# Optimization experiments

Hardware: AMD Instinct MI355X
Metric: run time of the kernel (lower is better)

## Reference

```python
import jax, jax.numpy as jnp
import numpy as np

B, D, H, O, E, R, K, NH = 2048, 512, 2048, 512, 8, 4, 2, 8
DH = O // NH
EPS = 1e-5

def _ln(x, g, b):
    m = x.mean(-1, keepdims=True)
    v = ((x - m) ** 2).mean(-1, keepdims=True)
    return (x - m) / jnp.sqrt(v + EPS) * g + b

def setup_inputs():
    key = jax.random.key(0)
    ks = jax.random.split(key, 16)
    n = lambda k, shape, fan: jax.random.normal(k, shape, jnp.float32) * (fan ** -0.5)
    x = jax.random.normal(ks[0], (B, D), jnp.float32)
    regime = jax.random.randint(ks[1], (B,), 0, R)
    regime_features = jax.nn.one_hot(regime, R, dtype=jnp.float32)
    return dict(
        x=x, regime=regime, regime_features=regime_features,
        ew1=n(ks[2], (R, E, D, H), D), eb1=jnp.zeros((R, E, H)),
        lng=jnp.ones((R, E, H)), lnb=jnp.zeros((R, E, H)),
        ew2=n(ks[3], (R, E, H, O), H), eb2=jnp.zeros((R, E, O)),
        rw1=n(ks[4], (R, D + R, H), D + R), rb1=jnp.zeros((R, H)),
        rw2=n(ks[5], (R, H, E), H), rb2=jnp.zeros((R, E)),
        ipw=n(ks[6], (3 * O, O), O), ipb=jnp.zeros((3 * O,)),
        opw=n(ks[7], (O, O), O), opb=jnp.zeros((O,)),
        ang=jnp.ones((O,)), anb=jnp.zeros((O,)),
    )

def _forward(x, regime, regime_features, ew1, eb1, lng, lnb, ew2, eb2, rw1, rb1, rw2, rb2, ipw, ipb, opw, opb, ang, anb):
    B_ = x.shape[0]
    bi = jnp.arange(B_)
    # regime-conditioned routing: compute logits for all regimes densely, select per sample
    ri = jnp.concatenate([x, regime_features], axis=-1)                  # [B, D+R]
    rh = jax.nn.relu(jnp.einsum('bf,rfh->rbh', ri, rw1) + rb1[:, None])
    logits = (jnp.einsum('rbh,rhe->rbe', rh, rw2) + rb2[:, None])[regime, bi]  # [B, E]
    w = jax.nn.softmax(logits, axis=-1)
    tkw, tki = jax.lax.top_k(w, K)
    tkw = tkw / tkw.sum(-1, keepdims=True)
    # experts: all regimes x all experts, then select the per-sample regime block
    h = jnp.einsum('bd,redh->rebh', x, ew1) + eb1[:, :, None]            # [R, E, B, H]
    h = jax.nn.relu(_ln(h, lng[:, :, None], lnb[:, :, None]))
    eo = jnp.einsum('rebh,reho->rebo', h, ew2) + eb2[:, :, None] + x[None, None]  # identity residual (D == O)
    eo = eo.transpose(0, 2, 1, 3)[regime, bi]                            # [B, E, O]
    # group attention over expert axis (torch MultiheadAttention, eval mode)
    qkv = eo @ ipw.T + ipb
    q, k, v = jnp.split(qkv, 3, axis=-1)
    sh = lambda t: t.reshape(B_, E, NH, DH).transpose(0, 2, 1, 3)
    q, k, v = sh(q), sh(k), sh(v)
    attn = jax.nn.softmax(jnp.einsum('bhqd,bhkd->bhqk', q, k) / np.sqrt(DH).astype(np.float32), axis=-1)
    av = jnp.einsum('bhqk,bhkd->bhqd', attn, v).transpose(0, 2, 1, 3).reshape(B_, E, O)
    eo = _ln(eo + av @ opw.T + opb, ang, anb)
    # top-k combine
    gathered = jnp.take_along_axis(eo, tki[:, :, None], axis=1)          # [B, K, O]
    return jnp.sum(tkw[:, :, None] * gathered, axis=1)

def reference(x, regime, regime_features, ew1, eb1, lng, lnb, ew2, eb2, rw1, rb1, rw2, rb2, ipw, ipb, opw, opb, ang, anb):
    return _forward(x, regime, regime_features, ew1, eb1, lng, lnb, ew2, eb2, rw1, rb1, rw2, rb2, ipw, ipb, opw, opb, ang, anb)
```

## Files before the change

kernel.cpp:

```cpp
#include <hip/hip_runtime.h>
#include <hip/hip_bf16.h>
#include <cstddef>

typedef __attribute__((ext_vector_type(8))) short short8;
typedef __attribute__((ext_vector_type(4))) float f32x4;

constexpr int CB = 2048;
constexpr int CD = 512;
constexpr int CH = 2048;
constexpr int CO = 512;
constexpr int CE = 8;
constexpr int CR = 4;

__device__ __forceinline__ float bs2f(short s){
  union { float f; unsigned u; } u; u.u = ((unsigned)(unsigned short)s) << 16; return u.f;
}
__device__ __forceinline__ short f2bs(float x){
  union { __hip_bfloat16 h; short s; } u; u.h = __float2bfloat16(x); return u.s;
}

#define GLL(g, l) __builtin_amdgcn_global_load_lds((const __attribute__((address_space(1))) void*)(g), (__attribute__((address_space(3))) void*)(l), 16, 0, 0)

__device__ __forceinline__ void block_reduce2(float& a, float& b){
#pragma unroll
  for (int off = 32; off; off >>= 1){ a += __shfl_xor(a, off, 64); b += __shfl_xor(b, off, 64); }
  __shared__ float sa[4], sb[4];
  const int wid = threadIdx.x >> 6, lane = threadIdx.x & 63;
  __syncthreads();
  if (lane == 0){ sa[wid] = a; sb[wid] = b; }
  __syncthreads();
  a = sa[0] + sa[1] + sa[2] + sa[3];
  b = sb[0] + sb[1] + sb[2] + sb[3];
}

__global__ void k_count(const int* __restrict__ regime, int* __restrict__ meta){
  int b = blockIdx.x * 256 + threadIdx.x;
  if (b < CB) atomicAdd(&meta[8 + regime[b]], 1);
}
__global__ void k_scan(int* meta){
  if (threadIdx.x == 0){
    int c0 = meta[8], c1 = meta[9], c2 = meta[10], c3 = meta[11];
    meta[0] = 0; meta[1] = c0; meta[2] = c0 + c1; meta[3] = c0 + c1 + c2; meta[4] = c0 + c1 + c2 + c3;
  }
}
__global__ void k_scatter(const int* __restrict__ regime, int* __restrict__ meta, int* __restrict__ perm){
  int b = blockIdx.x * 256 + threadIdx.x;
  if (b < CB){
    int r = regime[b];
    int pos = atomicAdd(&meta[12 + r], 1);
    perm[meta[r] + pos] = b;
  }
}

__global__ __launch_bounds__(256) void k_xsplit(const float* __restrict__ x, const int* __restrict__ perm,
                                                short* __restrict__ xp, short* __restrict__ xd){
  const int i = blockIdx.x;
  const int b = perm[i];
  const int c = threadIdx.x * 2;
  float2 v = *(const float2*)(x + (size_t)b * CD + c);
  short2 hi; hi.x = f2bs(v.x); hi.y = f2bs(v.y);
  short2 lo; lo.x = f2bs(v.x - bs2f(hi.x)); lo.y = f2bs(v.y - bs2f(hi.y));
  *(short2*)(xp + (size_t)i * CD + c) = hi;
  short* row = xd + (size_t)i * 2048;
  *(short2*)(row + c) = hi;
  *(short2*)(row + 512 + c) = hi;
  *(short2*)(row + 1024 + c) = lo;
  *(short2*)(row + 1536 + c) = lo;
}

__global__ __launch_bounds__(256) void k_cvt(const float* __restrict__ in, short* __restrict__ outp, int n){
  int i = (blockIdx.x * 256 + threadIdx.x) * 8;
  if (i >= n) return;
  float4 a = *(const float4*)(in + i);
  float4 b = *(const float4*)(in + i + 4);
  short8 o;
  o[0]=f2bs(a.x); o[1]=f2bs(a.y); o[2]=f2bs(a.z); o[3]=f2bs(a.w);
  o[4]=f2bs(b.x); o[5]=f2bs(b.y); o[6]=f2bs(b.z); o[7]=f2bs(b.w);
  *(short8*)(outp + i) = o;
}

__global__ __launch_bounds__(256) void k_cvt_t(const float* __restrict__ in, short* __restrict__ outp, int K, int N){
  __shared__ float tile[64][65];
  const int z = blockIdx.z;
  const int k0 = blockIdx.y * 64, n0 = blockIdx.x * 64;
  const float* src = in + (size_t)z * K * N;
  short* dst = outp + (size_t)z * K * N;
  const int t = threadIdx.x;
  const int kk = t >> 4, nq = (t & 15) * 4;
#pragma unroll
  for (int j = 0; j < 4; j++){
    float4 v = *(const float4*)(src + (size_t)(k0 + kk + j * 16) * N + n0 + nq);
    tile[kk + j * 16][nq] = v.x; tile[kk + j * 16][nq + 1] = v.y;
    tile[kk + j * 16][nq + 2] = v.z; tile[kk + j * 16][nq + 3] = v.w;
  }
  __syncthreads();
  const int n = t >> 2, kq = (t & 3) * 16;
  short8 o0, o1;
#pragma unroll
  for (int j = 0; j < 8; j++) o0[j] = f2bs(tile[kq + j][n]);
#pragma unroll
  for (int j = 0; j < 8; j++) o1[j] = f2bs(tile[kq + 8 + j][n]);
  short* drow = dst + (size_t)(n0 + n) * K + k0 + kq;
  *(short8*)(drow) = o0;
  *(short8*)(drow + 8) = o1;
}

__global__ __launch_bounds__(256) void k_rwt(const float* __restrict__ rw1, short* __restrict__ Bp){
  __shared__ float tile[64][65];
  const int r = blockIdx.z;
  const int k0 = blockIdx.y * 64, n0 = blockIdx.x * 64;
  const float* src = rw1 + (size_t)r * (CD + CR) * CH;
  short* dst = Bp + (size_t)r * CH * 2048;
  const int t = threadIdx.x;
  const int kk = t >> 4, nq = (t & 15) * 4;
#pragma unroll
  for (int j = 0; j < 4; j++){
    float4 v = *(const float4*)(src + (size_t)(k0 + kk + j * 16) * CH + n0 + nq);
    tile[kk + j * 16][nq] = v.x; tile[kk + j * 16][nq + 1] = v.y;
    tile[kk + j * 16][nq + 2] = v.z; tile[kk + j * 16][nq + 3] = v.w;
  }
  __syncthreads();
  const int n = t >> 2, kq = (t & 3) * 16;
  short8 h0, h1, l0, l1;
#pragma unroll
  for (int j = 0; j < 8; j++){
    float f = tile[kq + j][n];
    short h = f2bs(f); h0[j] = h; l0[j] = f2bs(f - bs2f(h));
  }
#pragma unroll
  for (int j = 0; j < 8; j++){
    float f = tile[kq + 8 + j][n];
    short h = f2bs(f); h1[j] = h; l1[j] = f2bs(f - bs2f(h));
  }
  short* drow = dst + (size_t)(n0 + n) * 2048;
  *(short8*)(drow + k0 + kq) = h0;        *(short8*)(drow + k0 + kq + 8) = h1;
  *(short8*)(drow + 512 + k0 + kq) = l0;  *(short8*)(drow + 512 + k0 + kq + 8) = l1;
  *(short8*)(drow + 1024 + k0 + kq) = h0; *(short8*)(drow + 1024 + k0 + kq + 8) = h1;
  *(short8*)(drow + 1536 + k0 + kq) = l0; *(short8*)(drow + 1536 + k0 + kq + 8) = l1;
}

__global__ void k_rbias(const float* __restrict__ rw1, const float* __restrict__ rb1, float* __restrict__ rbias){
  const int r = blockIdx.y, n = blockIdx.x * 256 + threadIdx.x;
  rbias[r * CH + n] = rb1[(size_t)r * CH + n] + rw1[((size_t)r * (CD + CR) + CD + r) * CH + n];
}

__global__ __launch_bounds__(256) void k_logits2(
    const float* __restrict__ part, const float* __restrict__ rb2,
    const int* __restrict__ meta, const int* __restrict__ perm,
    int* __restrict__ tki, float* __restrict__ tkw){
  const int wid = threadIdx.x >> 6, lane = threadIdx.x & 63;
  const int i = blockIdx.x * 4 + wid;
  const int r = (i >= meta[1]) + (i >= meta[2]) + (i >= meta[3]);
  const int p0 = lane >> 3, e = lane & 7;
  float v = 0.f;
#pragma unroll
  for (int j = 0; j < 4; j++)
    v += part[((size_t)(p0 + 8 * j) * CB + i) * 8 + e];
  v += __shfl_xor(v, 8, 64);
  v += __shfl_xor(v, 16, 64);
  v += __shfl_xor(v, 32, 64);
  v += rb2[r * CE + e];
  float l8[8];
#pragma unroll
  for (int e2 = 0; e2 < 8; e2++) l8[e2] = __shfl(v, e2, 64);
  if (lane == 0){
    int i1 = 0; float m1 = l8[0];
#pragma unroll
    for (int e2 = 1; e2 < 8; e2++) if (l8[e2] > m1){ m1 = l8[e2]; i1 = e2; }
    int i2 = -1; float m2 = -1e30f;
#pragma unroll
    for (int e2 = 0; e2 < 8; e2++) if (e2 != i1 && l8[e2] > m2){ m2 = l8[e2]; i2 = e2; }
    const float e2w = __expf(m2 - m1);
    const float w1 = 1.f / (1.f + e2w);
    const int b = perm[i];
    tki[b * 2] = i1; tki[b * 2 + 1] = i2;
    tkw[b * 2] = w1; tkw[b * 2 + 1] = e2w * w1;
  }
}
__global__ void k_qrows(const int* __restrict__ tki, int* __restrict__ qrows){
  int i = blockIdx.x * 256 + threadIdx.x;
  if (i < CB * 2) qrows[i] = (i >> 1) * CE + tki[i];
}

template<int EPI, bool SWZ>
__global__ __launch_bounds__(256) void gemm_bf16(
    const short* __restrict__ A, long lda,
    const short* __restrict__ Wt, long ldw,
    const int* __restrict__ goff, int fixedM, int Ksub, int ksplit, int N,
    const float* __restrict__ bias, long bstride,
    short* __restrict__ outb, short* __restrict__ outb2, float* __restrict__ outf,
    const int* __restrict__ operm, const float* __restrict__ xtra, int mbs, int nbs){
  constexpr int BK = 32;
  __shared__ __align__(16) short lds[2][8192];

  int bx, by, bz;
  if constexpr (SWZ){
    const int s = blockIdx.x;
    const int chunk = gridDim.x >> 3;
    const int l = (s & 7) * chunk + (s >> 3);
    bx = l % nbs; const int t2 = l / nbs; by = t2 % mbs; bz = t2 / mbs;
  } else { bx = blockIdx.x; by = blockIdx.y; bz = blockIdx.z; }

  const int ks = bz % ksplit;
  const int z = bz / ksplit;
  int g0 = 0, Mg = fixedM;
  if (goff){ const int r = (EPI == 6) ? z : (z >> 3); g0 = goff[r]; Mg = goff[r + 1] - g0; }
  const int m0 = by * 128;
  if (m0 >= Mg) return;
  const int n0 = bx * 128;
  const int e = z & 7;
  const long kbase = (long)ks * Ksub;

  const short* Ab;
  if constexpr (EPI == 2) Ab = A + ((size_t)e * CB + g0) * (size_t)lda;
  else if constexpr (EPI == 1 || EPI == 6) Ab = A + (size_t)g0 * (size_t)lda;
  else Ab = A;
  const short* Wb = Wt + (size_t)z * (size_t)N * (size_t)ldw;

  const int tid = threadIdx.x;
  const int lane = tid & 63, wid = tid >> 6;
  const int srow = lane >> 2;
  const int sc = (((lane & 3) ^ ((srow >> 1) & 3)) << 3);

  int ar0 = m0 + wid * 32 + srow;
  int ar1 = ar0 + 16;
  if (ar0 > Mg - 1) ar0 = Mg - 1;
  if (ar1 > Mg - 1) ar1 = Mg - 1;
  if constexpr (EPI == 3){
    if (operm){ ar0 = operm[ar0]; ar1 = operm[ar1]; }
  }
  const short* ga0 = Ab + (size_t)ar0 * lda + kbase + sc;
  const short* ga1 = Ab + (size_t)ar1 * lda + kbase + sc;
  const int brow = n0 + wid * 32 + srow;
  const short* gb0 = Wb + (size_t)brow * ldw + kbase + sc;
  const short* gb1 = gb0 + (size_t)16 * ldw;

  const int wm = (wid >> 1) * 64, wn = (wid & 1) * 64;
  const int r16 = lane & 15, kb = lane >> 4;
  const int rsw = (r16 >> 1) & 3;

  f32x4 acc[4][4];
#pragma unroll
  for (int a = 0; a < 4; a++)
#pragma unroll
    for (int b = 0; b < 4; b++) acc[a][b] = (f32x4){0.f, 0.f, 0.f, 0.f};

  const int NT = Ksub / BK;
  int buf = 0;

  {
    short* dA = &lds[0][0] + wid * 1024;
    short* dB = &lds[0][4096] + wid * 1024;
    GLL(ga0, dA); GLL(ga1, dA + 512);
    GLL(gb0, dB); GLL(gb1, dB + 512);
  }
  __syncthreads();

  for (int t = 0; t < NT; ++t){
    if (t + 1 < NT){
      const int kof = (t + 1) * BK;
      short* dA = &lds[buf ^ 1][0] + wid * 1024;
      short* dB = &lds[buf ^ 1][4096] + wid * 1024;
      GLL(ga0 + kof, dA); GLL(ga1 + kof, dA + 512);
      GLL(gb0 + kof, dB); GLL(gb1 + kof, dB + 512);
    }
    const short* sA = &lds[buf][0];
    const short* sB = &lds[buf][4096];
    short8 af[4], bfv[4];
#pragma unroll
    for (int mi = 0; mi < 4; mi++)
      af[mi] = *(const short8*)(sA + (wm + mi * 16 + r16) * 32 + ((kb ^ rsw) << 3));
#pragma unroll
    for (int ni = 0; ni < 4; ni++)
      bfv[ni] = *(const short8*)(sB + (wn + ni * 16 + r16) * 32 + ((kb ^ rsw) << 3));
#pragma unroll
    for (int mi = 0; mi < 4; mi++)
#pragma unroll
      for (int ni = 0; ni < 4; ni++)
        acc[mi][ni] = __builtin_amdgcn_mfma_f32_16x16x32_bf16(af[mi], bfv[ni], acc[mi][ni], 0, 0, 0);
    __syncthreads();
    buf ^= 1;
  }

  if constexpr (EPI == 6){
    const int hbase = n0 + wn;
    float wv[4][8]; float rbv[4];
#pragma unroll
    for (int ni = 0; ni < 4; ni++){
      const int h = hbase + ni * 16 + r16;
      rbv[ni] = bias[(size_t)z * CH + h];
      const float* wp = xtra + ((size_t)z * CH + h) * 8;
#pragma unroll
      for (int e2 = 0; e2 < 8; e2++) wv[ni][e2] = wp[e2];
    }
    const int slot = bx * 2 + (wid & 1);
#pragma unroll
    for (int mi = 0; mi < 4; mi++){
#pragma unroll
      for (int q = 0; q < 4; q++){
        float tmp[8];
#pragma unroll
        for (int e2 = 0; e2 < 8; e2++) tmp[e2] = 0.f;
#pragma unroll
        for (int ni = 0; ni < 4; ni++){
          const float v = fmaxf(acc[mi][ni][q] + rbv[ni], 0.f);
#pragma unroll
          for (int e2 = 0; e2 < 8; e2++) tmp[e2] += v * wv[ni][e2];
        }
#pragma unroll
        for (int e2 = 0; e2 < 8; e2++){
          tmp[e2] += __shfl_xor(tmp[e2], 1, 64);
          tmp[e2] += __shfl_xor(tmp[e2], 2, 64);
          tmp[e2] += __shfl_xor(tmp[e2], 4, 64);
          tmp[e2] += __shfl_xor(tmp[e2], 8, 64);
        }
        const int row = wm + mi * 16 + kb * 4 + q;
        if (r16 == 0 && m0 + row < Mg){
          float* dp = outf + ((size_t)slot * CB + (g0 + m0 + row)) * 8;
#pragma unroll
          for (int e2 = 0; e2 < 8; e2++) dp[e2] = tmp[e2];
        }
      }
    }
    return;
  }

#pragma unroll
  for (int mi = 0; mi < 4; mi++){
#pragma unroll
    for (int q = 0; q < 4; q++){
      const int i = m0 + wm + mi * 16 + kb * 4 + q;
      if (i >= Mg) continue;
#pragma unroll
      for (int ni = 0; ni < 4; ni++){
        const int n = n0 + wn + ni * 16 + r16;
        float v = acc[mi][ni][q];
        if constexpr (EPI == 1){
          v += bias[(size_t)z * bstride + n];
          outb[((size_t)e * CB + (g0 + i)) * (size_t)N + n] = f2bs(v);
        } else if constexpr (EPI == 2){
          const int borig = operm[g0 + i];
          short* tgt = ks ? outb2 : outb;
          tgt[((size_t)borig * CE + e) * (size_t)CO + n] = f2bs(v);
        } else if constexpr (EPI == 3){
          v += bias[n];
          outb[(size_t)i * (size_t)N + n] = f2bs(v);
        } else {
          v += bias[n];
          outf[(size_t)i * (size_t)N + n] = v;
        }
      }
    }
  }
}

__global__ __launch_bounds__(256) void k_eo(const short* __restrict__ p1,
    const float* __restrict__ eb2, const float* __restrict__ x, const int* __restrict__ regime,
    short* __restrict__ eo){
  const int b = blockIdx.x, e = blockIdx.y;
  const int r = regime[b];
  const int c = threadIdx.x * 2;
  const size_t idx = (((size_t)b * CE + e) << 9) + c;
  short2 a = *(const short2*)(eo + idx);
  short2 bb = *(const short2*)(p1 + idx);
  float2 xr = *(const float2*)(x + (size_t)b * CD + c);
  float2 eb = *(const float2*)(eb2 + (((size_t)r * CE + e) << 9) + c);
  short2 o;
  o.x = f2bs(bs2f(a.x) + bs2f(bb.x) + xr.x + eb.x);
  o.y = f2bs(bs2f(a.y) + bs2f(bb.y) + xr.y + eb.y);
  *(short2*)(eo + idx) = o;
}

__global__ __launch_bounds__(256) void k_ln(short* __restrict__ hact,
    const float* __restrict__ lng, const float* __restrict__ lnb, const int* __restrict__ meta){
  const int rowid = blockIdx.x;
  const int e = rowid >> 11, i = rowid & (CB - 1);
  const int r = (i >= meta[1]) + (i >= meta[2]) + (i >= meta[3]);
  short* p = hact + (size_t)rowid * CH;
  short8 raw = *(short8*)(p + threadIdx.x * 8);
  float v[8]; float s = 0.f, sq = 0.f;
#pragma unroll
  for (int j = 0; j < 8; j++){ v[j] = bs2f(raw[j]); s += v[j]; sq += v[j] * v[j]; }
  block_reduce2(s, sq);
  const float mean = s * (1.f / CH);
  const float var = sq * (1.f / CH) - mean * mean;
  const float rstd = rsqrtf(fmaxf(var, 0.f) + 1e-5f);
  const float* g = lng + ((size_t)r * CE + e) * CH;
  const float* bb = lnb + ((size_t)r * CE + e) * CH;
  short8 outv;
#pragma unroll
  for (int j = 0; j < 8; j++){
    const int h = threadIdx.x * 8 + j;
    const float val = (v[j] - mean) * rstd * g[h] + bb[h];
    outv[j] = f2bs(fmaxf(val, 0.f));
  }
  *(short8*)(p + threadIdx.x * 8) = outv;
}

__global__ __launch_bounds__(128) void k_attn(const short* __restrict__ qb, const short* __restrict__ kv,
    const int* __restrict__ tki, short* __restrict__ av){
  const int b = blockIdx.x;
  const int j = threadIdx.x >> 6, d = threadIdx.x & 63;
  const short* q = qb + (size_t)(b * 2 + j) * CO;
  const short* base = kv + (size_t)b * CE * 1024;
#pragma unroll
  for (int h = 0; h < 8; h++){
    const float qv = bs2f(q[h * 64 + d]);
    float sc[8];
#pragma unroll
    for (int e = 0; e < 8; e++){
      float pp = qv * bs2f(base[(size_t)e * 1024 + h * 64 + d]);
#pragma unroll
      for (int off = 32; off; off >>= 1) pp += __shfl_xor(pp, off, 64);
      sc[e] = pp * 0.125f;
    }
    float m = sc[0];
#pragma unroll
    for (int e = 1; e < 8; e++) m = fmaxf(m, sc[e]);
    float den = 0.f, avd = 0.f;
#pragma unroll
    for (int e = 0; e < 8; e++){
      const float pe = __expf(sc[e] - m);
      den += pe;
      avd += pe * bs2f(base[(size_t)e * 1024 + 512 + h * 64 + d]);
    }
    av[((size_t)b * 2 + j) * CO + h * 64 + d] = f2bs(avd / den);
  }
}

__global__ __launch_bounds__(256) void k_final(const short* __restrict__ eo,
    const float* __restrict__ proj, const int* __restrict__ tki, const float* __restrict__ tkw,
    const float* __restrict__ ang, const float* __restrict__ anb, float* __restrict__ out){
  const int b = blockIdx.x, t = threadIdx.x;
  float o0 = 0.f, o1 = 0.f;
#pragma unroll
  for (int j = 0; j < 2; j++){
    const int s = tki[b * 2 + j];
    const float w = tkw[b * 2 + j];
    const short* ep = eo + ((size_t)b * CE + s) * CO;
    const float* pp = proj + ((size_t)b * 2 + j) * CO;
    const float v0 = bs2f(ep[t]) + pp[t];
    const float v1 = bs2f(ep[t + 256]) + pp[t + 256];
    float sm = v0 + v1, sq = v0 * v0 + v1 * v1;
    block_reduce2(sm, sq);
    const float mean = sm * (1.f / CO);
    const float rstd = rsqrtf(fmaxf(sq * (1.f / CO) - mean * mean, 0.f) + 1e-5f);
    o0 += w * ((v0 - mean) * rstd * ang[t] + anb[t]);
    o1 += w * ((v1 - mean) * rstd * ang[t + 256] + anb[t + 256]);
  }
  out[(size_t)b * CO + t] = o0;
  out[(size_t)b * CO + t + 256] = o1;
}

extern "C" void kernel_launch(void* const* d_in, const int* in_sizes, int n_in,
                              void* d_out, int out_size, void* d_ws, size_t ws_size,
                              hipStream_t stream){
  const float* x    = (const float*)d_in[0];
  const int*   regime = (const int*)d_in[1];
  const float* ew1  = (const float*)d_in[3];
  const float* eb1  = (const float*)d_in[4];
  const float* lng  = (const float*)d_in[5];
  const float* lnb  = (const float*)d_in[6];
  const float* ew2  = (const float*)d_in[7];
  const float* eb2  = (const float*)d_in[8];
  const float* rw1  = (const float*)d_in[9];
  const float* rb1  = (const float*)d_in[10];
  const float* rw2  = (const float*)d_in[11];
  const float* rb2  = (const float*)d_in[12];
  const float* ipw  = (const float*)d_in[13];
  const float* ipb  = (const float*)d_in[14];
  const float* opw  = (const float*)d_in[15];
  const float* opb  = (const float*)d_in[16];
  const float* ang  = (const float*)d_in[17];
  const float* anb  = (const float*)d_in[18];
  float* out = (float*)d_out;

  char* ws = (char*)d_ws;
  int*   meta  = (int*)(ws);
  int*   perm  = (int*)(ws + (16u << 10));
  int*   tki   = (int*)(ws + (32u << 10));
  float* tkw   = (float*)(ws + (48u << 10));
  int*   qrows = (int*)(ws + (64u << 10));
  float* rbias = (float*)(ws + (80u << 10));
  short* ipwb  = (short*)(ws + (256u << 10));
  short* opwb  = (short*)(ws + (1792u << 10));
  short* xp    = (short*)(ws + (2304u << 10));
  short* eo    = (short*)(ws + (4352u << 10));
  short* hact  = (short*)(ws + (22ull << 20));
  short* qkv   = (short*)(ws + (22ull << 20));
  short* qb    = (short*)(ws + (54ull << 20));
  short* av    = (short*)(ws + (58ull << 20));
  float* proj  = (float*)(ws + (62ull << 20));
  float* part  = (float*)(ws + (70ull << 20));
  short* wt    = (short*)(ws + (86ull << 20));
  short* xd    = (short*)(ws + (150ull << 20));
  short* p1    = (short*)(ws + (150ull << 20));

  hipMemsetAsync(meta, 0, 1024, stream);
  k_count  <<<8, 256, 0, stream>>>(regime, meta);
  k_scan   <<<1, 64, 0, stream>>>(meta);
  k_scatter<<<8, 256, 0, stream>>>(regime, meta, perm);
  k_xsplit <<<CB, 256, 0, stream>>>(x, perm, xp, xd);
  k_cvt    <<<384, 256, 0, stream>>>(ipw, ipwb, 1536 * 512);
  k_cvt    <<<128, 256, 0, stream>>>(opw, opwb, 512 * 512);

  k_rwt  <<<dim3(32, 8, CR), 256, 0, stream>>>(rw1, wt);
  k_rbias<<<dim3(8, CR), 256, 0, stream>>>(rw1, rb1, rbias);
  gemm_bf16<6, false><<<dim3(16, 16, CR), 256, 0, stream>>>(
      xd, 2048, wt, 2048, meta, 0, 2048, 1, CH, rbias, 0,
      nullptr, nullptr, part, nullptr, rw2, 0, 0);
  k_logits2<<<CB / 4, 256, 0, stream>>>(part, rb2, meta, perm, tki, tkw);
  k_qrows<<<16, 256, 0, stream>>>(tki, qrows);

  k_cvt_t<<<dim3(32, 8, 32), 256, 0, stream>>>(ew1, wt, CD, CH);
  gemm_bf16<1, true><<<8192, 256, 0, stream>>>(
      xp, CD, wt, CD, meta, 0, CD, 1, CH, eb1, CH, hact, nullptr, nullptr, nullptr, nullptr, 16, 16);
  k_ln<<<CE * CB, 256, 0, stream>>>(hact, lng, lnb, meta);

  k_cvt_t<<<dim3(8, 32, 32), 256, 0, stream>>>(ew2, wt, CH, CO);
  gemm_bf16<2, true><<<4096, 256, 0, stream>>>(
      hact, CH, wt, CH, meta, 0, 1024, 2, CO, nullptr, 0, eo, p1, nullptr, perm, nullptr, 16, 4);
  k_eo<<<dim3(CB, CE), 256, 0, stream>>>(p1, eb2, x, regime, eo);

  gemm_bf16<3, true><<<1024, 256, 0, stream>>>(
      eo, CO, ipwb + (size_t)512 * 512, CO, nullptr, CB * CE, CO, 1, 1024, ipb + 512, 0,
      qkv, nullptr, nullptr, nullptr, nullptr, 128, 8);
  gemm_bf16<3, false><<<dim3(4, 32, 1), 256, 0, stream>>>(
      eo, CO, ipwb, CO, nullptr, CB * 2, CO, 1, CO, ipb, 0,
      qb, nullptr, nullptr, qrows, nullptr, 0, 0);

  k_attn<<<CB, 128, 0, stream>>>(qb, qkv, tki, av);

  gemm_bf16<4, false><<<dim3(4, 32, 1), 256, 0, stream>>>(
      av, CO, opwb, CO, nullptr, CB * 2, CO, 1, CO, opb, 0,
      nullptr, nullptr, proj, nullptr, nullptr, 0, 0);

  k_final<<<CB, 256, 0, stream>>>(eo, proj, tki, tkw, ang, anb, out);
  (void)in_sizes; (void)n_in; (void)out_size; (void)ws_size;
}
```

Before: 441.2 us.

## Drop lo*lo split term in router GEMM, split-K 4 for expert GEMM2, fuse small kernels

The router GEMM's split-bf16 emulation shrinks from four terms to three by dropping the lo*lo product, so K goes from 2048 to 1536. The second expert GEMM now uses split-K of 4 instead of 2, and all partials go to separate buffers that k_eo sums. Several small launches are merged: the two weight casts become one kernel, the bias computation moves into k_rwt, and qrows is written in k_logits2. This saves GEMM work and launches but writes and reads more partial-sum traffic, and slightly lowers router precision.

```diff
diff --git a/kernel.cpp b/kernel.cpp
--- a/kernel.cpp
+++ b/kernel.cpp
@@ -61,22 +61,24 @@
   short2 hi; hi.x = f2bs(v.x); hi.y = f2bs(v.y);
   short2 lo; lo.x = f2bs(v.x - bs2f(hi.x)); lo.y = f2bs(v.y - bs2f(hi.y));
   *(short2*)(xp + (size_t)i * CD + c) = hi;
-  short* row = xd + (size_t)i * 2048;
+  short* row = xd + (size_t)i * 1536;
   *(short2*)(row + c) = hi;
   *(short2*)(row + 512 + c) = hi;
   *(short2*)(row + 1024 + c) = lo;
-  *(short2*)(row + 1536 + c) = lo;
-}
-
-__global__ __launch_bounds__(256) void k_cvt(const float* __restrict__ in, short* __restrict__ outp, int n){
+}
+
+__global__ __launch_bounds__(256) void k_cvt2(const float* __restrict__ a, short* __restrict__ ao, int na,
+                                              const float* __restrict__ b, short* __restrict__ bo, int nb){
   int i = (blockIdx.x * 256 + threadIdx.x) * 8;
-  if (i >= n) return;
-  float4 a = *(const float4*)(in + i);
-  float4 b = *(const float4*)(in + i + 4);
+  const float* src; short* dst;
+  if (i < na){ src = a + i; dst = ao + i; }
+  else { int j = i - na; if (j >= nb) return; src = b + j; dst = bo + j; }
+  float4 u = *(const float4*)(src);
+  float4 v = *(const float4*)(src + 4);
   short8 o;
-  o[0]=f2bs(a.x); o[1]=f2bs(a.y); o[2]=f2bs(a.z); o[3]=f2bs(a.w);
-  o[4]=f2bs(b.x); o[5]=f2bs(b.y); o[6]=f2bs(b.z); o[7]=f2bs(b.w);
-  *(short8*)(outp + i) = o;
+  o[0]=f2bs(u.x); o[1]=f2bs(u.y); o[2]=f2bs(u.z); o[3]=f2bs(u.w);
+  o[4]=f2bs(v.x); o[5]=f2bs(v.y); o[6]=f2bs(v.z); o[7]=f2bs(v.w);
+  *(short8*)(dst) = o;
 }
 
 __global__ __launch_bounds__(256) void k_cvt_t(const float* __restrict__ in, short* __restrict__ outp, int K, int N){
@@ -105,13 +107,18 @@
   *(short8*)(drow + 8) = o1;
 }
 
-__global__ __launch_bounds__(256) void k_rwt(const float* __restrict__ rw1, short* __restrict__ Bp){
+__global__ __launch_bounds__(256) void k_rwt(const float* __restrict__ rw1, const float* __restrict__ rb1,
+                                             short* __restrict__ Bp, float* __restrict__ rbias){
   __shared__ float tile[64][65];
   const int r = blockIdx.z;
   const int k0 = blockIdx.y * 64, n0 = blockIdx.x * 64;
   const float* src = rw1 + (size_t)r * (CD + CR) * CH;
-  short* dst = Bp + (size_t)r * CH * 2048;
+  short* dst = Bp + (size_t)r * CH * 1536;
   const int t = threadIdx.x;
+  if (blockIdx.y == 0 && t < 64){
+    const int n = n0 + t;
+    rbias[r * CH + n] = rb1[(size_t)r * CH + n] + src[((size_t)(CD + r)) * CH + n];
+  }
   const int kk = t >> 4, nq = (t & 15) * 4;
 #pragma unroll
   for (int j = 0; j < 4; j++){
@@ -132,22 +139,16 @@
     float f = tile[kq + 8 + j][n];
     short h = f2bs(f); h1[j] = h; l1[j] = f2bs(f - bs2f(h));
   }
-  short* drow = dst + (size_t)(n0 + n) * 2048;
+  short* drow = dst + (size_t)(n0 + n) * 1536;
   *(short8*)(drow + k0 + kq) = h0;        *(short8*)(drow + k0 + kq + 8) = h1;
   *(short8*)(drow + 512 + k0 + kq) = l0;  *(short8*)(drow + 512 + k0 + kq + 8) = l1;
   *(short8*)(drow + 1024 + k0 + kq) = h0; *(short8*)(drow + 1024 + k0 + kq + 8) = h1;
-  *(short8*)(drow + 1536 + k0 + kq) = l0; *(short8*)(drow + 1536 + k0 + kq + 8) = l1;
-}
-
-__global__ void k_rbias(const float* __restrict__ rw1, const float* __restrict__ rb1, float* __restrict__ rbias){
-  const int r = blockIdx.y, n = blockIdx.x * 256 + threadIdx.x;
-  rbias[r * CH + n] = rb1[(size_t)r * CH + n] + rw1[((size_t)r * (CD + CR) + CD + r) * CH + n];
 }
 
 __global__ __launch_bounds__(256) void k_logits2(
     const float* __restrict__ part, const float* __restrict__ rb2,
     const int* __restrict__ meta, const int* __restrict__ perm,
-    int* __restrict__ tki, float* __restrict__ tkw){
+    int* __restrict__ tki, float* __restrict__ tkw, int* __restrict__ qrows){
   const int wid = threadIdx.x >> 6, lane = threadIdx.x & 63;
   const int i = blockIdx.x * 4 + wid;
   const int r = (i >= meta[1]) + (i >= meta[2]) + (i >= meta[3]);
@@ -175,11 +176,8 @@
     const int b = perm[i];
     tki[b * 2] = i1; tki[b * 2 + 1] = i2;
     tkw[b * 2] = w1; tkw[b * 2 + 1] = e2w * w1;
-  }
-}
-__global__ void k_qrows(const int* __restrict__ tki, int* __restrict__ qrows){
-  int i = blockIdx.x * 256 + threadIdx.x;
-  if (i < CB * 2) qrows[i] = (i >> 1) * CE + tki[i];
+    qrows[b * 2] = b * CE + i1; qrows[b * 2 + 1] = b * CE + i2;
+  }
 }
 
 template<int EPI, bool SWZ>
@@ -188,7 +186,7 @@
     const short* __restrict__ Wt, long ldw,
     const int* __restrict__ goff, int fixedM, int Ksub, int ksplit, int N,
     const float* __restrict__ bias, long bstride,
-    short* __restrict__ outb, short* __restrict__ outb2, float* __restrict__ outf,
+    short* __restrict__ outb, float* __restrict__ outf,
     const int* __restrict__ operm, const float* __restrict__ xtra, int mbs, int nbs){
   constexpr int BK = 32;
   __shared__ __align__(16) short lds[2][8192];
@@ -340,8 +338,7 @@
           outb[((size_t)e * CB + (g0 + i)) * (size_t)N + n] = f2bs(v);
         } else if constexpr (EPI == 2){
           const int borig = operm[g0 + i];
-          short* tgt = ks ? outb2 : outb;
-          tgt[((size_t)borig * CE + e) * (size_t)CO + n] = f2bs(v);
+          outb[(size_t)ks * bstride + ((size_t)borig * CE + e) * (size_t)CO + n] = f2bs(v);
         } else if constexpr (EPI == 3){
           v += bias[n];
           outb[(size_t)i * (size_t)N + n] = f2bs(v);
@@ -354,20 +351,22 @@
   }
 }
 
-__global__ __launch_bounds__(256) void k_eo(const short* __restrict__ p1,
+__global__ __launch_bounds__(256) void k_eo(const short* __restrict__ P, long pstr,
     const float* __restrict__ eb2, const float* __restrict__ x, const int* __restrict__ regime,
     short* __restrict__ eo){
   const int b = blockIdx.x, e = blockIdx.y;
   const int r = regime[b];
   const int c = threadIdx.x * 2;
   const size_t idx = (((size_t)b * CE + e) << 9) + c;
-  short2 a = *(const short2*)(eo + idx);
-  short2 bb = *(const short2*)(p1 + idx);
+  short2 a0 = *(const short2*)(P + idx);
+  short2 a1 = *(const short2*)(P + pstr + idx);
+  short2 a2 = *(const short2*)(P + 2 * pstr + idx);
+  short2 a3 = *(const short2*)(P + 3 * pstr + idx);
   float2 xr = *(const float2*)(x + (size_t)b * CD + c);
   float2 eb = *(const float2*)(eb2 + (((size_t)r * CE + e) << 9) + c);
   short2 o;
-  o.x = f2bs(bs2f(a.x) + bs2f(bb.x) + xr.x + eb.x);
-  o.y = f2bs(bs2f(a.y) + bs2f(bb.y) + xr.y + eb.y);
+  o.x = f2bs(bs2f(a0.x) + bs2f(a1.x) + bs2f(a2.x) + bs2f(a3.x) + xr.x + eb.x);
+  o.y = f2bs(bs2f(a0.y) + bs2f(a1.y) + bs2f(a2.y) + bs2f(a3.y) + xr.y + eb.y);
   *(short2*)(eo + idx) = o;
 }
 
@@ -493,47 +492,45 @@
   float* proj  = (float*)(ws + (62ull << 20));
   float* part  = (float*)(ws + (70ull << 20));
   short* wt    = (short*)(ws + (86ull << 20));
-  short* xd    = (short*)(ws + (150ull << 20));
-  short* p1    = (short*)(ws + (150ull << 20));
+  short* P     = (short*)(ws + (150ull << 20));
+  short* xd    = (short*)(ws + (216ull << 20));
+  const long PSTR = (long)CB * CE * CO;
 
   hipMemsetAsync(meta, 0, 1024, stream);
   k_count  <<<8, 256, 0, stream>>>(regime, meta);
   k_scan   <<<1, 64, 0, stream>>>(meta);
   k_scatter<<<8, 256, 0, stream>>>(regime, meta, perm);
   k_xsplit <<<CB, 256, 0, stream>>>(x, perm, xp, xd);
-  k_cvt    <<<384, 256, 0, stream>>>(ipw, ipwb, 1536 * 512);
-  k_cvt    <<<128, 256, 0, stream>>>(opw, opwb, 512 * 512);
-
-  k_rwt  <<<dim3(32, 8, CR), 256, 0, stream>>>(rw1, wt);
-  k_rbias<<<dim3(8, CR), 256, 0, stream>>>(rw1, rb1, rbias);
+  k_cvt2   <<<512, 256, 0, stream>>>(ipw, ipwb, 1536 * 512, opw, opwb, 512 * 512);
+
+  k_rwt<<<dim3(32, 8, CR), 256, 0, stream>>>(rw1, rb1, wt, rbias);
   gemm_bf16<6, false><<<dim3(16, 16, CR), 256, 0, stream>>>(
-      xd, 2048, wt, 2048, meta, 0, 2048, 1, CH, rbias, 0,
-      nullptr, nullptr, part, nullptr, rw2, 0, 0);
-  k_logits2<<<CB / 4, 256, 0, stream>>>(part, rb2, meta, perm, tki, tkw);
-  k_qrows<<<16, 256, 0, stream>>>(tki, qrows);
+      xd, 1536, wt, 1536, meta, 0, 1536, 1, CH, rbias, 0,
+      nullptr, part, nullptr, rw2, 0, 0);
+  k_logits2<<<CB / 4, 256, 0, stream>>>(part, rb2, meta, perm, tki, tkw, qrows);
 
   k_cvt_t<<<dim3(32, 8, 32), 256, 0, stream>>>(ew1, wt, CD, CH);
   gemm_bf16<1, true><<<8192, 256, 0, stream>>>(
-      xp, CD, wt, CD, meta, 0, CD, 1, CH, eb1, CH, hact, nullptr, nullptr, nullptr, nullptr, 16, 16);
+      xp, CD, wt, CD, meta, 0, CD, 1, CH, eb1, CH, hact, nullptr, nullptr, nullptr, 16, 16);
   k_ln<<<CE * CB, 256, 0, stream>>>(hact, lng, lnb, meta);
 
   k_cvt_t<<<dim3(8, 32, 32), 256, 0, stream>>>(ew2, wt, CH, CO);
-  gemm_bf16<2, true><<<4096, 256, 0, stream>>>(
-      hact, CH, wt, CH, meta, 0, 1024, 2, CO, nullptr, 0, eo, p1, nullptr, perm, nullptr, 16, 4);
-  k_eo<<<dim3(CB, CE), 256, 0, stream>>>(p1, eb2, x, regime, eo);
+  gemm_bf16<2, true><<<8192, 256, 0, stream>>>(
+      hact, CH, wt, CH, meta, 0, 512, 4, CO, nullptr, PSTR, P, nullptr, perm, nullptr, 16, 4);
+  k_eo<<<dim3(CB, CE), 256, 0, stream>>>(P, PSTR, eb2, x, regime, eo);
 
   gemm_bf16<3, true><<<1024, 256, 0, stream>>>(
       eo, CO, ipwb + (size_t)512 * 512, CO, nullptr, CB * CE, CO, 1, 1024, ipb + 512, 0,
-      qkv, nullptr, nullptr, nullptr, nullptr, 128, 8);
+      qkv, nullptr, nullptr, nullptr, 128, 8);
   gemm_bf16<3, false><<<dim3(4, 32, 1), 256, 0, stream>>>(
       eo, CO, ipwb, CO, nullptr, CB * 2, CO, 1, CO, ipb, 0,
-      qb, nullptr, nullptr, qrows, nullptr, 0, 0);
+      qb, nullptr, qrows, nullptr, 0, 0);
 
   k_attn<<<CB, 128, 0, stream>>>(qb, qkv, tki, av);
 
   gemm_bf16<4, false><<<dim3(4, 32, 1), 256, 0, stream>>>(
       av, CO, opwb, CO, nullptr, CB * 2, CO, 1, CO, opb, 0,
-      nullptr, nullptr, proj, nullptr, nullptr, 0, 0);
+      nullptr, proj, nullptr, nullptr, 0, 0);
 
   k_final<<<CB, 256, 0, stream>>>(eo, proj, tki, tkw, ang, anb, out);
   (void)in_sizes; (void)n_in; (void)out_size; (void)ws_size;
```

Result: no change. 449.1 us (+1.8%).
